# Performance work log

Hardware: AMD Instinct MI355X
Metric: run time of the kernel (lower is better)

The kernel has to match this reference:

```python
import jax, jax.numpy as jnp
import numpy as np

NUM_RBF = 16
RBF_D_MIN, RBF_D_MAX = 2.0, 22.0
CB_A, CB_B, CB_C = -0.58273431, 0.56802827, -0.54067466
TOP_K = 32
MAX_REL = 32
NPOS = 16
HID = 128
LN_EPS = 1e-5


def _gather_nodes(nodes, idx):
    # nodes: (B, L, D), idx: (B, L, K) -> (B, L, K, D)
    return jax.vmap(lambda n, i: n[i])(nodes, idx)


def _rbf_encode(D):
    mu = jnp.linspace(RBF_D_MIN, RBF_D_MAX, NUM_RBF, dtype=D.dtype)
    sigma = (RBF_D_MAX - RBF_D_MIN) / NUM_RBF
    return jnp.exp(-((D[..., None] - mu) ** 2) / (sigma ** 2))


def setup_inputs() -> dict:
    key = jax.random.key(0)
    ks = jax.random.split(key, 4)
    B, L = 2, 2048
    X = jax.random.normal(ks[0], (B, L, 4, 3), jnp.float32) * 10.0
    residue_mask = jnp.ones((B, L), jnp.float32)
    R_idx = jnp.arange(B * L, dtype=jnp.int32).reshape(B, L)
    chain_labels = jnp.zeros((B, L), jnp.int32)
    # learned params
    W_pos = jax.random.normal(ks[1], (NPOS, 2 * MAX_REL + 2), jnp.float32) * 0.05
    b_pos = jnp.zeros((NPOS,), jnp.float32)
    W_edge = jax.random.normal(ks[2], (HID, 25 * NUM_RBF + NPOS), jnp.float32) * 0.02
    ln_gamma = jnp.ones((HID,), jnp.float32)
    ln_beta = jnp.zeros((HID,), jnp.float32)
    return {"X": X, "residue_mask": residue_mask, "R_idx": R_idx,
            "chain_labels": chain_labels, "W_pos": W_pos, "b_pos": b_pos,
            "W_edge": W_edge, "ln_gamma": ln_gamma, "ln_beta": ln_beta}


def reference(X, residue_mask, R_idx, chain_labels, W_pos, b_pos, W_edge, ln_gamma, ln_beta):
    B, L = X.shape[0], X.shape[1]
    K = min(TOP_K, L)
    # virtual CB from backbone N, CA, C
    N, CA, C = X[..., 0, :], X[..., 1, :], X[..., 2, :]
    b = CA - N
    c = C - CA
    a = jnp.cross(b, c, axis=-1)
    CB = (CB_A * a + CB_B * b + CB_C * c + CA)[..., None, :]
    atoms_5 = jnp.concatenate([X, CB], axis=-2)  # (B, L, 5, 3)
    # kNN on CA coords with invalid residues pushed far away
    diff = CA[:, :, None, :] - CA[:, None, :, :]
    dist_sq = jnp.sum(diff * diff, axis=-1)  # (B, L, L)
    inv_mask = 1.0 - residue_mask
    dist_sq = dist_sq + inv_mask[:, None, :] * 1e6
    _, E_idx = jax.lax.top_k(-dist_sq, K)  # smallest-k indices, (B, L, K)
    # gather neighbor 5-atom coords and compute 25 pairwise distances
    Xf = atoms_5.reshape(B, L, 15)
    Xg = _gather_nodes(Xf, E_idx).reshape(B, L, K, 5, 3)
    d2 = jnp.sum((atoms_5[:, :, None, :, None, :] - Xg[:, :, :, None, :, :]) ** 2, axis=-1)
    D = jnp.sqrt(d2 + 1e-6)  # (B, L, K, 5, 5)
    rbf = _rbf_encode(D).reshape(B, L, K, 25 * NUM_RBF)
    # positional encodings (standard ProteinMPNN form)
    Rg = _gather_nodes(R_idx[..., None], E_idx)[..., 0]  # (B, L, K)
    Cg = _gather_nodes(chain_labels[..., None], E_idx)[..., 0]
    d_rel = Rg - R_idx[:, :, None]
    same_chain = (Cg == chain_labels[:, :, None])
    d_clip = jnp.clip(d_rel + MAX_REL, 0, 2 * MAX_REL)
    d_final = jnp.where(same_chain, d_clip, 2 * MAX_REL + 1)
    oh = jax.nn.one_hot(d_final, 2 * MAX_REL + 2, dtype=rbf.dtype)
    pos_enc = jnp.einsum('blkc,pc->blkp', oh, W_pos) + b_pos
    # edge embedding + layernorm
    edge_input = jnp.concatenate([pos_enc, rbf], axis=-1)  # (B, L, K, 416)
    h = jnp.einsum('blkf,hf->blkh', edge_input, W_edge)
    mean = jnp.mean(h, axis=-1, keepdims=True)
    var = jnp.var(h, axis=-1, keepdims=True)
    E = (h - mean) * jax.lax.rsqrt(var + LN_EPS) * ln_gamma + ln_beta
    return E_idx, E
```

## Files before the change

kernel.cpp:

```cpp
#include <hip/hip_runtime.h>
#include <hip/hip_bf16.h>

#define LEN   2048
#define KNB   32
#define HID   128
#define FS    512

typedef unsigned long long ull;
typedef unsigned int uint32;
typedef float f32x4  __attribute__((ext_vector_type(4)));
typedef float f32x16 __attribute__((ext_vector_type(16)));

__device__ __forceinline__ void bar_lgkm() {
    asm volatile("s_waitcnt lgkmcnt(0)" ::: "memory");
    __builtin_amdgcn_s_barrier();
    asm volatile("" ::: "memory");
}

__global__ __launch_bounds__(256) void prep_kernel(
    const float* __restrict__ X, const float* __restrict__ mask,
    const float* __restrict__ W_edge,
    float4* __restrict__ CAm, int* __restrict__ Wf8) {
    const int t = blockIdx.x * 256 + threadIdx.x;
    if (t < 2 * LEN) {
        const float* p = X + (size_t)t * 12;
        CAm[t] = make_float4(p[3], p[4], p[5],
                             __fmul_rn(__fsub_rn(1.0f, mask[t]), 1000000.0f));
    }
    if (t < 13312) {
        const float4 w = ((const float4*)W_edge)[t];
        int r = __builtin_amdgcn_cvt_pk_fp8_f32(w.x, w.y, 0, false);
        r = __builtin_amdgcn_cvt_pk_fp8_f32(w.z, w.w, r, true);
        Wf8[t] = r;
    }
}

__global__ __launch_bounds__(256) void topk_kernel(
    const float4* __restrict__ CAm, float* __restrict__ eidx_out) {
    const int row = blockIdx.x;
    const int b = row >> 11;
    const int i = row & (LEN - 1);
    const int tid = threadIdx.x;

    __shared__ int hist[512];
    __shared__ ull cand[LEN];
    __shared__ int candcnt;
    __shared__ int selB;

    const float4* C = CAm + (size_t)b * LEN;
    const float4 ci = C[i];

    uint32 d2b[8];
#pragma unroll
    for (int q = 0; q < 8; ++q) {
        const float4 cj = C[q * 256 + tid];
        float dx = __fsub_rn(ci.x, cj.x);
        float dy = __fsub_rn(ci.y, cj.y);
        float dz = __fsub_rn(ci.z, cj.z);
        float d2 = __fadd_rn(__fadd_rn(__fmul_rn(dx, dx), __fmul_rn(dy, dy)),
                             __fmul_rn(dz, dz));
        d2 = __fadd_rn(d2, cj.w);
        d2b[q] = __float_as_uint(d2);
    }

    hist[tid] = 0; hist[tid + 256] = 0;
    if (tid == 0) candcnt = 0;
    __syncthreads();
#pragma unroll
    for (int q = 0; q < 8; ++q) atomicAdd(&hist[d2b[q] >> 22], 1);
    __syncthreads();

    if (tid < 64) {
        int loc[8];
        int s = 0;
#pragma unroll
        for (int t = 0; t < 8; ++t) { loc[t] = hist[tid * 8 + t]; s += loc[t]; }
        int incl = s;
#pragma unroll
        for (int off = 1; off < 64; off <<= 1) {
            int o = __shfl_up(incl, off, 64);
            if (tid >= off) incl += o;
        }
        const int excl = incl - s;
        if (excl < KNB && incl >= KNB) {
            int c = excl;
#pragma unroll
            for (int t = 0; t < 8; ++t) {
                int c2 = c + loc[t];
                if (c < KNB && c2 >= KNB) selB = tid * 8 + t;
                c = c2;
            }
        }
    }
    __syncthreads();
    const uint32 B = (uint32)selB;

#pragma unroll
    for (int q = 0; q < 8; ++q) {
        if ((d2b[q] >> 22) <= B) {
            int p = atomicAdd(&candcnt, 1);
            cand[p] = (((ull)d2b[q]) << 32) | (uint32)(q * 256 + tid);
        }
    }
    __syncthreads();
    const int M = candcnt;

    for (int c = tid; c < M; c += 256) {
        const ull k = cand[c];
        int r = 0;
        for (int m = 0; m < M; ++m) r += (cand[m] < k);
        if (r < KNB)
            eidx_out[(size_t)row * KNB + r] = (float)(uint32)(k & 0xFFFFFFFFull);
    }
}

__device__ __forceinline__ void load_res_atoms(const float* __restrict__ p, float* dst) {
    const float Nx = p[0], Ny = p[1], Nz = p[2];
    const float Ax = p[3], Ay = p[4], Az = p[5];
    const float Cx = p[6], Cy = p[7], Cz = p[8];
    const float Ox = p[9], Oy = p[10], Oz = p[11];
    const float bx = Ax - Nx, by = Ay - Ny, bz = Az - Nz;
    const float cx = Cx - Ax, cy = Cy - Ay, cz = Cz - Az;
    const float axv = by * cz - bz * cy;
    const float ayv = bz * cx - bx * cz;
    const float azv = bx * cy - by * cx;
    dst[0] = Nx;  dst[1] = Ny;  dst[2] = Nz;
    dst[3] = Ax;  dst[4] = Ay;  dst[5] = Az;
    dst[6] = Cx;  dst[7] = Cy;  dst[8] = Cz;
    dst[9] = Ox;  dst[10] = Oy; dst[11] = Oz;
    dst[12] = -0.58273431f * axv + 0.56802827f * bx + -0.54067466f * cx + Ax;
    dst[13] = -0.58273431f * ayv + 0.56802827f * by + -0.54067466f * cy + Ay;
    dst[14] = -0.58273431f * azv + 0.56802827f * bz + -0.54067466f * cz + Az;
}

__device__ __forceinline__ int pk4(float a, float b, float c, float d) {
    int r = __builtin_amdgcn_cvt_pk_fp8_f32(a, b, 0, false);
    return __builtin_amdgcn_cvt_pk_fp8_f32(c, d, r, true);
}

#define E1  3.2053337e-1f
#define E3  3.2931300e-2f
#define E5  3.3834001e-3f
#define E7  3.4760500e-4f

__device__ __forceinline__ void compute_features(
    int tid, int Ri, int Ci,
    const float* __restrict__ wposL,
    const int* jR, const int* jC,
    const float (*natoms)[15], const float* iatoms,
    unsigned char* featF8) {
    {
        const int e = tid >> 4, p = tid & 15;
        const int drel = jR[e] - Ri;
        const int same = (jC[e] == Ci);
        int dc = drel + 32;
        dc = dc < 0 ? 0 : (dc > 64 ? 64 : dc);
        const int df = same ? dc : 65;
        const float v = wposL[p * 66 + df];
        const int pb = __builtin_amdgcn_cvt_pk_fp8_f32(v, 0.0f, 0, false);
        featF8[e * FS + ((e & 7) << 4) + p] = (unsigned char)(pb & 0xFF);
    }
#pragma unroll
    for (int it = 0; it < 2; ++it) {
        const int task = tid + it * 512;
        if (task < 800) {
            const int mn = task >> 5, e = task & 31;
            const int m = mn / 5, n = mn - m * 5;
            const float ax = iatoms[m * 3 + 0];
            const float ay = iatoms[m * 3 + 1];
            const float az = iatoms[m * 3 + 2];
            const float* na = &natoms[e][n * 3];
            const float dx = ax - na[0], dy = ay - na[1], dz = az - na[2];
            const float D = sqrtf(dx * dx + dy * dy + dz * dz + 1e-6f);
            const float Dc = fminf(D, 40.0f);
            const float v4 = Dc - 7.3333333f;
            const float A4  = __expf(-0.64f * v4 * v4);
            const float C4  = __expf(1.7066667f * v4);
            const float Ci4 = 1.0f / C4;
            int4 w4;
            {
                const float f3 = A4 * Ci4 * E1;
                const float f2 = f3 * Ci4 * E3;
                const float f1 = f2 * Ci4 * E5;
                const float f0 = f1 * Ci4 * E7;
                w4.x = pk4(f0, f1, f2, f3);
            }
            {
                const float f5 = A4 * C4 * E1;
                const float f6 = f5 * C4 * E3;
                const float f7 = f6 * C4 * E5;
                w4.y = pk4(A4, f5, f6, f7);
            }
            const float v12 = Dc - 18.0f;
            const float A12  = __expf(-0.64f * v12 * v12);
            const float C12  = C4 * 1.24140e-8f;
            const float Ci12 = Ci4 * 8.05543e7f;
            {
                const float f11 = A12 * Ci12 * E1;
                const float f10 = f11 * Ci12 * E3;
                const float f9  = f10 * Ci12 * E5;
                const float f8  = f9  * Ci12 * E7;
                w4.z = pk4(f8, f9, f10, f11);
            }
            {
                const float f13 = A12 * C12 * E1;
                const float f14 = f13 * C12 * E3;
                const float f15 = f14 * C12 * E5;
                w4.w = pk4(A12, f13, f14, f15);
            }
            *(int4*)(featF8 + e * FS + (((1 + mn) ^ (e & 7)) << 4)) = w4;
        }
    }
}

__global__ __launch_bounds__(512, 4) void edge_kernel(
    const float* __restrict__ X,
    const int* __restrict__ Ridx, const int* __restrict__ Chain,
    const float* __restrict__ W_pos, const float* __restrict__ b_pos,
    const unsigned char* __restrict__ Wf8,
    const float* __restrict__ lng, const float* __restrict__ lnb,
    const float* __restrict__ eidx_f, float* __restrict__ outE) {
    const int tid = threadIdx.x;
    const int row0 = blockIdx.x * 8;
    const int b = row0 >> 11;
    const int i0 = row0 & (LEN - 1);

    __shared__ __align__(16) unsigned char featF8[2][32 * FS];
    __shared__ float natoms[8][32][15];
    __shared__ float iatoms[8][16];
    __shared__ float wposL[16 * 66];
    __shared__ __align__(16) float pS[2][32][4], pQ[2][32][4];
    __shared__ float gbuf[HID], bbuf[HID];
    __shared__ int jR[8][KNB], jC[8][KNB];
    __shared__ int riS[8], ciS[8];

    const float* Xb = X + (size_t)b * LEN * 12;

    const int w = tid >> 6, l = tid & 63;
    const int rowsel = w >> 2, cg = w & 3;
    const int e32 = l & 31, hi = l >> 5;

    long wreg[26];
    {
        const unsigned char* wb = Wf8 + (size_t)(cg * 32 + e32) * 416 + hi * 8;
#pragma unroll
        for (int ks = 0; ks < 26; ++ks)
            wreg[ks] = *(const long*)(wb + ks * 16);
    }

    for (int t = tid; t < 1056; t += 512)
        wposL[t] = W_pos[t] + b_pos[t / 66];
    if (tid < 256) {
        const int r = tid >> 5, e = tid & 31;
        const int j = (int)eidx_f[(size_t)(row0 + r) * KNB + e];
        jR[r][e] = Ridx[b * LEN + j];
        jC[r][e] = Chain[b * LEN + j];
        load_res_atoms(Xb + j * 12, &natoms[r][e][0]);
    } else if (tid < 264) {
        const int r = tid - 256;
        load_res_atoms(Xb + (size_t)(i0 + r) * 12, &iatoms[r][0]);
    } else if (tid < 272) {
        riS[tid - 264] = Ridx[b * LEN + i0 + (tid - 264)];
    } else if (tid < 280) {
        ciS[tid - 272] = Chain[b * LEN + i0 + (tid - 272)];
    } else if (tid >= 384) {
        const int t2 = tid - 384;
        gbuf[t2] = lng[t2];
        bbuf[t2] = lnb[t2];
    }
    bar_lgkm();

    compute_features(tid, riS[0], ciS[0], wposL, jR[0], jC[0],
                     natoms[0], iatoms[0], featF8[0]);
    compute_features(tid, riS[1], ciS[1], wposL, jR[1], jC[1],
                     natoms[1], iatoms[1], featF8[1]);
    bar_lgkm();

    for (int it = 0; it < 4; ++it) {
        const int myrow = row0 + 2 * it + rowsel;

        f32x16 acc = {0.f, 0.f, 0.f, 0.f, 0.f, 0.f, 0.f, 0.f,
                      0.f, 0.f, 0.f, 0.f, 0.f, 0.f, 0.f, 0.f};
        {
            const unsigned char* fb = featF8[rowsel] + e32 * FS + hi * 8;
            const int sw = e32 & 7;
#pragma unroll
            for (int ks = 0; ks < 26; ++ks) {
                const long a = *(const long*)(fb + ((ks ^ sw) << 4));
                acc = __builtin_amdgcn_mfma_f32_32x32x16_fp8_fp8(wreg[ks], a, acc, 0, 0, 0);
            }
        }
        {
            float s = 0.f, q = 0.f;
#pragma unroll
            for (int r = 0; r < 16; ++r) { s += acc[r]; q += acc[r] * acc[r]; }
            s += __shfl_xor(s, 32, 64);
            q += __shfl_xor(q, 32, 64);
            if (hi == 0) {
                pS[rowsel][e32][cg] = s;
                pQ[rowsel][e32][cg] = q;
            }
        }
        bar_lgkm();

        {
            const float4 ps = *(const float4*)&pS[rowsel][e32][0];
            const float4 pq = *(const float4*)&pQ[rowsel][e32][0];
            const float s = ps.x + ps.y + ps.z + ps.w;
            const float q = pq.x + pq.y + pq.z + pq.w;
            const float mean = s * (1.0f / 128.0f);
            const float rstd = rsqrtf(q * (1.0f / 128.0f) - mean * mean + 1e-5f);
            const int cb = cg * 32 + hi * 4;
            float* orow = outE + ((size_t)myrow * KNB + e32) * HID + cb;
#pragma unroll
            for (int j = 0; j < 4; ++j) {
                const float4 gg = *(const float4*)&gbuf[cb + 8 * j];
                const float4 bb = *(const float4*)&bbuf[cb + 8 * j];
                float4 o;
                o.x = (acc[4 * j + 0] - mean) * rstd * gg.x + bb.x;
                o.y = (acc[4 * j + 1] - mean) * rstd * gg.y + bb.y;
                o.z = (acc[4 * j + 2] - mean) * rstd * gg.z + bb.z;
                o.w = (acc[4 * j + 3] - mean) * rstd * gg.w + bb.w;
                *(float4*)(orow + 8 * j) = o;
            }
        }
        if (it < 3) {
            const int na = 2 * it + 2, nb = 2 * it + 3;
            compute_features(tid, riS[na], ciS[na], wposL, jR[na], jC[na],
                             natoms[na], iatoms[na], featF8[0]);
            compute_features(tid, riS[nb], ciS[nb], wposL, jR[nb], jC[nb],
                             natoms[nb], iatoms[nb], featF8[1]);
        }
        bar_lgkm();
    }
}

extern "C" void kernel_launch(void* const* d_in, const int* in_sizes, int n_in,
                              void* d_out, int out_size, void* d_ws, size_t ws_size,
                              hipStream_t stream) {
    const float* X      = (const float*)d_in[0];
    const float* mask   = (const float*)d_in[1];
    const int*   Ridx   = (const int*)d_in[2];
    const int*   Chain  = (const int*)d_in[3];
    const float* W_pos  = (const float*)d_in[4];
    const float* b_pos  = (const float*)d_in[5];
    const float* W_edge = (const float*)d_in[6];
    const float* lng    = (const float*)d_in[7];
    const float* lnb    = (const float*)d_in[8];

    float* out  = (float*)d_out;
    float* eidx = out;
    float* E    = out + (size_t)2 * LEN * KNB;

    float4* CAm = (float4*)d_ws;
    unsigned char* Wf8 = (unsigned char*)d_ws + 2 * LEN * 16;

    const int nrow = 2 * LEN;
    prep_kernel<<<52, 256, 0, stream>>>(X, mask, W_edge, CAm, (int*)Wf8);
    topk_kernel<<<nrow, 256, 0, stream>>>(CAm, eidx);
    edge_kernel<<<nrow / 8, 512, 0, stream>>>(X, Ridx, Chain, W_pos, b_pos, Wf8,
                                              lng, lnb, eidx, E);
}
```

Before: 59.95 us.

## Fold prep kernel into topk kernel and replace XOR swizzle with padded feature rows

Removes the separate prep launch. Extra blocks appended to the topk grid now do the fp8 conversion of W_edge, and each topk block reads CA coordinates and the mask straight from X instead of a precomputed float4 array. The edge kernel's fp8 feature buffer drops the XOR swizzle and instead pads each row stride from 512 to 520 bytes to avoid LDS bank conflicts, writing with two 8-byte stores. This saves one kernel launch and one round trip through global memory, but topk now does strided 12-float loads of X per element, which may fetch less efficiently.

```diff
diff --git a/kernel.cpp b/kernel.cpp
--- a/kernel.cpp
+++ b/kernel.cpp
@@ -4,7 +4,7 @@
 #define LEN   2048
 #define KNB   32
 #define HID   128
-#define FS    512
+#define FS    520
 
 typedef unsigned long long ull;
 typedef unsigned int uint32;
@@ -17,49 +17,49 @@
     asm volatile("" ::: "memory");
 }
 
-__global__ __launch_bounds__(256) void prep_kernel(
+__global__ __launch_bounds__(256) void topk_kernel(
     const float* __restrict__ X, const float* __restrict__ mask,
-    const float* __restrict__ W_edge,
-    float4* __restrict__ CAm, int* __restrict__ Wf8) {
-    const int t = blockIdx.x * 256 + threadIdx.x;
-    if (t < 2 * LEN) {
-        const float* p = X + (size_t)t * 12;
-        CAm[t] = make_float4(p[3], p[4], p[5],
-                             __fmul_rn(__fsub_rn(1.0f, mask[t]), 1000000.0f));
-    }
-    if (t < 13312) {
-        const float4 w = ((const float4*)W_edge)[t];
-        int r = __builtin_amdgcn_cvt_pk_fp8_f32(w.x, w.y, 0, false);
-        r = __builtin_amdgcn_cvt_pk_fp8_f32(w.z, w.w, r, true);
-        Wf8[t] = r;
-    }
-}
-
-__global__ __launch_bounds__(256) void topk_kernel(
-    const float4* __restrict__ CAm, float* __restrict__ eidx_out) {
-    const int row = blockIdx.x;
+    const float* __restrict__ W_edge, int* __restrict__ Wf8,
+    float* __restrict__ eidx_out) {
+    const int bid = blockIdx.x;
+    const int tid = threadIdx.x;
+
+    if (bid >= 2 * LEN) {
+        const int t = (bid - 2 * LEN) * 256 + tid;
+        if (t < 13312) {
+            const float4 w = ((const float4*)W_edge)[t];
+            int r = __builtin_amdgcn_cvt_pk_fp8_f32(w.x, w.y, 0, false);
+            r = __builtin_amdgcn_cvt_pk_fp8_f32(w.z, w.w, r, true);
+            Wf8[t] = r;
+        }
+        return;
+    }
+
+    const int row = bid;
     const int b = row >> 11;
     const int i = row & (LEN - 1);
-    const int tid = threadIdx.x;
 
     __shared__ int hist[512];
     __shared__ ull cand[LEN];
     __shared__ int candcnt;
     __shared__ int selB;
 
-    const float4* C = CAm + (size_t)b * LEN;
-    const float4 ci = C[i];
+    const float* Xb = X + (size_t)b * LEN * 12;
+    const float* mb = mask + (size_t)b * LEN;
+    const float cax = Xb[i * 12 + 3];
+    const float cay = Xb[i * 12 + 4];
+    const float caz = Xb[i * 12 + 5];
 
     uint32 d2b[8];
 #pragma unroll
     for (int q = 0; q < 8; ++q) {
-        const float4 cj = C[q * 256 + tid];
-        float dx = __fsub_rn(ci.x, cj.x);
-        float dy = __fsub_rn(ci.y, cj.y);
-        float dz = __fsub_rn(ci.z, cj.z);
+        const int j = q * 256 + tid;
+        float dx = __fsub_rn(cax, Xb[j * 12 + 3]);
+        float dy = __fsub_rn(cay, Xb[j * 12 + 4]);
+        float dz = __fsub_rn(caz, Xb[j * 12 + 5]);
         float d2 = __fadd_rn(__fadd_rn(__fmul_rn(dx, dx), __fmul_rn(dy, dy)),
                              __fmul_rn(dz, dz));
-        d2 = __fadd_rn(d2, cj.w);
+        d2 = __fadd_rn(d2, __fmul_rn(__fsub_rn(1.0f, mb[j]), 1000000.0f));
         d2b[q] = __float_as_uint(d2);
     }
 
@@ -158,7 +158,7 @@
         const int df = same ? dc : 65;
         const float v = wposL[p * 66 + df];
         const int pb = __builtin_amdgcn_cvt_pk_fp8_f32(v, 0.0f, 0, false);
-        featF8[e * FS + ((e & 7) << 4) + p] = (unsigned char)(pb & 0xFF);
+        featF8[e * FS + p] = (unsigned char)(pb & 0xFF);
     }
 #pragma unroll
     for (int it = 0; it < 2; ++it) {
@@ -177,19 +177,17 @@
             const float A4  = __expf(-0.64f * v4 * v4);
             const float C4  = __expf(1.7066667f * v4);
             const float Ci4 = 1.0f / C4;
-            int4 w4;
+            ull lo, hi2;
             {
                 const float f3 = A4 * Ci4 * E1;
                 const float f2 = f3 * Ci4 * E3;
                 const float f1 = f2 * Ci4 * E5;
                 const float f0 = f1 * Ci4 * E7;
-                w4.x = pk4(f0, f1, f2, f3);
-            }
-            {
                 const float f5 = A4 * C4 * E1;
                 const float f6 = f5 * C4 * E3;
                 const float f7 = f6 * C4 * E5;
-                w4.y = pk4(A4, f5, f6, f7);
+                lo = (uint32)pk4(f0, f1, f2, f3)
+                   | ((ull)(uint32)pk4(A4, f5, f6, f7) << 32);
             }
             const float v12 = Dc - 18.0f;
             const float A12  = __expf(-0.64f * v12 * v12);
@@ -200,15 +198,14 @@
                 const float f10 = f11 * Ci12 * E3;
                 const float f9  = f10 * Ci12 * E5;
                 const float f8  = f9  * Ci12 * E7;
-                w4.z = pk4(f8, f9, f10, f11);
-            }
-            {
                 const float f13 = A12 * C12 * E1;
                 const float f14 = f13 * C12 * E3;
                 const float f15 = f14 * C12 * E5;
-                w4.w = pk4(A12, f13, f14, f15);
-            }
-            *(int4*)(featF8 + e * FS + (((1 + mn) ^ (e & 7)) << 4)) = w4;
+                hi2 = (uint32)pk4(f8, f9, f10, f11)
+                    | ((ull)(uint32)pk4(A12, f13, f14, f15) << 32);
+            }
+            *(ull*)(featF8 + e * FS + 16 + mn * 16)     = lo;
+            *(ull*)(featF8 + e * FS + 16 + mn * 16 + 8) = hi2;
         }
     }
 }
@@ -283,10 +280,9 @@
                       0.f, 0.f, 0.f, 0.f, 0.f, 0.f, 0.f, 0.f};
         {
             const unsigned char* fb = featF8[rowsel] + e32 * FS + hi * 8;
-            const int sw = e32 & 7;
 #pragma unroll
             for (int ks = 0; ks < 26; ++ks) {
-                const long a = *(const long*)(fb + ((ks ^ sw) << 4));
+                const long a = *(const long*)(fb + ks * 16);
                 acc = __builtin_amdgcn_mfma_f32_32x32x16_fp8_fp8(wreg[ks], a, acc, 0, 0, 0);
             }
         }
@@ -352,12 +348,10 @@
     float* eidx = out;
     float* E    = out + (size_t)2 * LEN * KNB;
 
-    float4* CAm = (float4*)d_ws;
-    unsigned char* Wf8 = (unsigned char*)d_ws + 2 * LEN * 16;
+    unsigned char* Wf8 = (unsigned char*)d_ws;
 
     const int nrow = 2 * LEN;
-    prep_kernel<<<52, 256, 0, stream>>>(X, mask, W_edge, CAm, (int*)Wf8);
-    topk_kernel<<<nrow, 256, 0, stream>>>(CAm, eidx);
+    topk_kernel<<<nrow + 52, 256, 0, stream>>>(X, mask, W_edge, (int*)Wf8, eidx);
     edge_kernel<<<nrow / 8, 512, 0, stream>>>(X, Ridx, Chain, W_pos, b_pos, Wf8,
                                               lng, lnb, eidx, E);
 }
```

New measurement: 54.70 us. 1.1x faster.
